# Kernel optimization log

Measured on AMD Instinct MI355X. Metric: run time of the kernel, lower is better.

## Reference

```python
import jax, jax.numpy as jnp
import numpy as np

NUM_PARTS = 2
SAMPLE_STEP = 3  # models sample_points(pts, 3, True) as deterministic stride-3 subsampling


def quat_to_rot(q):
    # wxyz quaternion -> 3x3 rotation (same formula as the torch module)
    q = q / jnp.linalg.norm(q)
    a, b, c, d = q[0], q[1], q[2], q[3]
    return jnp.stack([
        1 - 2 * c * c - 2 * d * d, 2 * b * c - 2 * a * d, 2 * a * c + 2 * b * d,
        2 * b * c + 2 * a * d, 1 - 2 * b * b - 2 * d * d, 2 * c * d - 2 * a * b,
        2 * b * d - 2 * a * c, 2 * a * b + 2 * c * d, 1 - 2 * b * b - 2 * c * c,
    ]).reshape(3, 3)


def make_transform(q, t):
    rot = quat_to_rot(q)                      # (3,3)
    top = jnp.concatenate([rot, t], axis=1)   # (3,4)
    bottom = jnp.array([[0.0, 0.0, 0.0, 1.0]], dtype=top.dtype)
    return jnp.concatenate([top, bottom], axis=0)  # (4,4)


def chamfer(x, y):
    # x: (M,4), y: (M,4) homogeneous points; symmetric chamfer of Euclidean cdist
    d2 = jnp.sum(x * x, -1)[:, None] + jnp.sum(y * y, -1)[None, :] - 2.0 * (x @ y.T)
    d = jnp.sqrt(jnp.maximum(d2, 0.0))
    return jnp.mean(jnp.min(d, axis=1)) + jnp.mean(jnp.min(d, axis=0))


def setup_inputs() -> dict:
    key = jax.random.key(0)
    ks = jax.random.split(key, 6)
    N = 24576
    camera_pts = jax.random.normal(ks[0], (NUM_PARTS, N, 3), dtype=jnp.float32)
    cad_pts = jax.random.normal(ks[1], (NUM_PARTS, N, 3), dtype=jnp.float32)
    part_weight = jax.random.uniform(ks[2], (NUM_PARTS + 1,), dtype=jnp.float32)
    rot_quat = jax.random.normal(ks[3], (NUM_PARTS, 4), dtype=jnp.float32)
    tra = jax.random.normal(ks[4], (NUM_PARTS, 3, 1), dtype=jnp.float32)
    joint_axes = jax.random.normal(ks[5], (NUM_PARTS, 2, 4), dtype=jnp.float32)
    return {"camera_pts": camera_pts, "cad_pts": cad_pts, "part_weight": part_weight,
            "rot_quat": rot_quat, "tra": tra, "joint_axes": joint_axes}


def reference(camera_pts, cad_pts, part_weight, rot_quat, tra, joint_axes):
    # stride-3 subsample, then homogenize with a ones column
    scad = cad_pts[:, ::SAMPLE_STEP]      # (P, M, 3)
    scam = camera_pts[:, ::SAMPLE_STEP]   # (P, M, 3)
    ones = jnp.ones(scad.shape[:-1] + (1,), dtype=scad.dtype)
    scad_h = jnp.concatenate([scad, ones], axis=-1)  # (P, M, 4)
    scam_h = jnp.concatenate([scam, ones], axis=-1)  # (P, M, 4)

    transforms = jax.vmap(make_transform)(rot_quat, tra)        # (P, 4, 4)
    cad_base = jnp.einsum('pij,pnj->pni', transforms, scad_h)   # (P, M, 4)

    e_geo_parts = jax.vmap(chamfer)(cad_base, scam_h)           # (P,)
    e_geo = jnp.dot(part_weight[:NUM_PARTS], e_geo_parts)

    diff = transforms[0] @ joint_axes[0].T - transforms[1] @ joint_axes[1].T  # (4, K)
    e_kin = jax.nn.sigmoid(-5.0 * jnp.linalg.norm(diff))

    all_objective = e_geo + part_weight[NUM_PARTS] * e_kin
    return all_objective, e_kin, jax.lax.stop_gradient(transforms)
```

## Files before the change

### kernel.cpp

```cpp
#include <hip/hip_runtime.h>
#include <math.h>

#define NS 8192
#define NPTS 24576
#define YSPLIT 16
#define YTILE 512
#define BX 256
#define XPT 4
#define XB (NS / (BX * XPT))


__global__ void prep_kernel(const float* __restrict__ rot_quat,
                            const float* __restrict__ tra,
                            const float* __restrict__ joint_axes,
                            float* __restrict__ ws, float* __restrict__ out) {
    if (threadIdx.x == 0) {
        float T[2][16];
        for (int p = 0; p < 2; ++p) {
            float a = rot_quat[p * 4 + 0], b = rot_quat[p * 4 + 1];
            float c = rot_quat[p * 4 + 2], d = rot_quat[p * 4 + 3];
            float inv = rsqrtf(a * a + b * b + c * c + d * d);
            a *= inv; b *= inv; c *= inv; d *= inv;
            float* t = T[p];
            t[0]  = 1.f - 2.f * c * c - 2.f * d * d;
            t[1]  = 2.f * b * c - 2.f * a * d;
            t[2]  = 2.f * a * c + 2.f * b * d;
            t[3]  = tra[p * 3 + 0];
            t[4]  = 2.f * b * c + 2.f * a * d;
            t[5]  = 1.f - 2.f * b * b - 2.f * d * d;
            t[6]  = 2.f * c * d - 2.f * a * b;
            t[7]  = tra[p * 3 + 1];
            t[8]  = 2.f * b * d - 2.f * a * c;
            t[9]  = 2.f * a * b + 2.f * c * d;
            t[10] = 1.f - 2.f * b * b - 2.f * c * c;
            t[11] = tra[p * 3 + 2];
            t[12] = 0.f; t[13] = 0.f; t[14] = 0.f; t[15] = 1.f;
            for (int k = 0; k < 16; ++k) {
                ws[4 + p * 16 + k] = t[k];
                out[2 + p * 16 + k] = t[k];
            }
        }
        float ss = 0.f;
        for (int i = 0; i < 4; ++i) {
            for (int j = 0; j < 2; ++j) {
                float d0 = 0.f, d1 = 0.f;
                for (int k = 0; k < 4; ++k) {
                    d0 += T[0][i * 4 + k] * joint_axes[0 * 8 + j * 4 + k];
                    d1 += T[1][i * 4 + k] * joint_axes[1 * 8 + j * 4 + k];
                }
                float df = d0 - d1;
                ss += df * df;
            }
        }
        float nrm = sqrtf(ss);
        float ek = 1.f / (1.f + expf(5.f * nrm));
        ws[36] = ek;
        out[1] = ek;
        ws[0] = 0.f; ws[1] = 0.f; ws[2] = 0.f; ws[3] = 0.f;
    }
}

__global__ void pack_kernel(const float* __restrict__ cam_pts,
                            const float* __restrict__ cad_pts,
                            const float* __restrict__ ws,
                            float4* __restrict__ pts) {
    int gid = blockIdx.x * blockDim.x + threadIdx.x;
    if (gid >= 2 * NS) return;
    int p = gid >> 13;
    int i = gid & (NS - 1);
    const float* T = ws + 4 + p * 16;
    int base = p * NPTS * 3 + i * 9;
    float x = cad_pts[base], y = cad_pts[base + 1], z = cad_pts[base + 2];
    float q0 = T[0] * x + T[1] * y + T[2]  * z + T[3];
    float q1 = T[4] * x + T[5] * y + T[6]  * z + T[7];
    float q2 = T[8] * x + T[9] * y + T[10] * z + T[11];
    pts[p * NS + i] = make_float4(q0, q1, q2, q0 * q0 + q1 * q1 + q2 * q2);
    float cx = cam_pts[base], cy = cam_pts[base + 1], cz = cam_pts[base + 2];
    pts[2 * NS + p * NS + i] = make_float4(cx, cy, cz, cx * cx + cy * cy + cz * cz);
}

__global__ __launch_bounds__(BX) void chamfer_kernel(const float4* __restrict__ pts,
                                                     float* __restrict__ partial) {
    int combo = blockIdx.y;
    int p   = combo >> 1;
    int dir = combo & 1;
    const float4* X = pts + (dir == 0 ? p * NS : 2 * NS + p * NS);
    const float4* Y = pts + (dir == 0 ? 2 * NS + p * NS : p * NS);
    int ys = blockIdx.z;
    int xb = blockIdx.x;

    __shared__ float4 sy[YTILE];

    int xbase = xb * (BX * XPT) + threadIdx.x;
    float m0[XPT], m1[XPT], m2[XPT], s[XPT], dmin[XPT];
#pragma unroll
    for (int k = 0; k < XPT; ++k) {
        float4 v = X[xbase + k * BX];
        m0[k] = -2.f * v.x;
        m1[k] = -2.f * v.y;
        m2[k] = -2.f * v.z;
        s[k]  = v.w;
        dmin[k] = 3.4e38f;
    }

    int ybase = ys * YTILE;
    sy[threadIdx.x]       = Y[ybase + threadIdx.x];
    sy[threadIdx.x + BX]  = Y[ybase + BX + threadIdx.x];
    __syncthreads();

#pragma unroll 4
    for (int j = 0; j < YTILE; ++j) {
        float4 y = sy[j];
#pragma unroll
        for (int k = 0; k < XPT; ++k) {
            float d = s[k] + y.w;
            d = fmaf(m0[k], y.x, d);
            d = fmaf(m1[k], y.y, d);
            d = fmaf(m2[k], y.z, d);
            dmin[k] = fminf(dmin[k], d);
        }
    }

#pragma unroll
    for (int k = 0; k < XPT; ++k) {
        partial[combo * (YSPLIT * NS) + ys * NS + xbase + k * BX] = dmin[k];
    }
}

__global__ void reduce_kernel(const float* __restrict__ partial,
                              float* __restrict__ accum) {
    int combo = blockIdx.y;
    int x = blockIdx.x * 256 + threadIdx.x;
    const float* p = partial + combo * (YSPLIT * NS) + x;
    float m = p[0];
#pragma unroll
    for (int ysi = 1; ysi < YSPLIT; ++ysi) m = fminf(m, p[ysi * NS]);
    float d = sqrtf(fmaxf(m, 0.f));
#pragma unroll
    for (int off = 32; off > 0; off >>= 1) d += __shfl_down(d, off, 64);
    __shared__ float sm[4];
    int wid = threadIdx.x >> 6;
    if ((threadIdx.x & 63) == 0) sm[wid] = d;
    __syncthreads();
    if (threadIdx.x == 0) {
        float sum = sm[0] + sm[1] + sm[2] + sm[3];
        atomicAdd(&accum[combo], sum);
    }
}

__global__ void finalize_kernel(const float* __restrict__ ws,
                                const float* __restrict__ pw,
                                float* __restrict__ out) {
    if (threadIdx.x == 0) {
        float e0 = (ws[0] + ws[1]) * (1.f / NS);
        float e1 = (ws[2] + ws[3]) * (1.f / NS);
        float e_geo = pw[0] * e0 + pw[1] * e1;
        out[0] = e_geo + pw[2] * ws[36];
    }
}

extern "C" void kernel_launch(void* const* d_in, const int* in_sizes, int n_in,
                              void* d_out, int out_size, void* d_ws, size_t ws_size,
                              hipStream_t stream) {
    const float* cam = (const float*)d_in[0];
    const float* cad = (const float*)d_in[1];
    const float* pw  = (const float*)d_in[2];
    const float* rq  = (const float*)d_in[3];
    const float* tr  = (const float*)d_in[4];
    const float* ja  = (const float*)d_in[5];
    float* out = (float*)d_out;
    float* ws  = (float*)d_ws;
    float4* pts = (float4*)(ws + 64);
    float* partial = ws + 64 + 16 * NS;

    prep_kernel<<<1, 64, 0, stream>>>(rq, tr, ja, ws, out);
    pack_kernel<<<(2 * NS) / 256, 256, 0, stream>>>(cam, cad, ws, pts);
    dim3 cg(XB, 4, YSPLIT);
    chamfer_kernel<<<cg, BX, 0, stream>>>(pts, partial);
    reduce_kernel<<<dim3(NS / 256, 4), 256, 0, stream>>>(partial, ws);
    finalize_kernel<<<1, 64, 0, stream>>>(ws, pw, out);
}
```

Measured before the change: 101.2 us.

## Fuse prep and pack into chamfer kernel and fold finalize into reduce

Drops the separate prep, pack and finalize launches. Each chamfer block now builds its transform itself, gathers the strided raw points directly, and applies the transform on the fly. The reduce kernel uses an atomic ticket counter so the last block writes the final objective. The inner loop also moves the x-norm term out of the per-pair distance and processes two y points per iteration. This cuts launch overhead and the round trip through global memory, at the cost of redundant transform and gather work in every block. The accumulators and ticket counter are zeroed in the fused kernel, so correctness depends on that kernel finishing before the reduce kernel starts, which stream ordering provides.

```diff
diff --git a/kernel.cpp b/kernel.cpp
--- a/kernel.cpp
+++ b/kernel.cpp
@@ -9,153 +9,163 @@
 #define XPT 4
 #define XB (NS / (BX * XPT))
 
+#define PARTIAL_OFF 131136
 
-__global__ void prep_kernel(const float* __restrict__ rot_quat,
-                            const float* __restrict__ tra,
-                            const float* __restrict__ joint_axes,
-                            float* __restrict__ ws, float* __restrict__ out) {
-    if (threadIdx.x == 0) {
-        float T[2][16];
-        for (int p = 0; p < 2; ++p) {
-            float a = rot_quat[p * 4 + 0], b = rot_quat[p * 4 + 1];
-            float c = rot_quat[p * 4 + 2], d = rot_quat[p * 4 + 3];
-            float inv = rsqrtf(a * a + b * b + c * c + d * d);
-            a *= inv; b *= inv; c *= inv; d *= inv;
-            float* t = T[p];
-            t[0]  = 1.f - 2.f * c * c - 2.f * d * d;
-            t[1]  = 2.f * b * c - 2.f * a * d;
-            t[2]  = 2.f * a * c + 2.f * b * d;
-            t[3]  = tra[p * 3 + 0];
-            t[4]  = 2.f * b * c + 2.f * a * d;
-            t[5]  = 1.f - 2.f * b * b - 2.f * d * d;
-            t[6]  = 2.f * c * d - 2.f * a * b;
-            t[7]  = tra[p * 3 + 1];
-            t[8]  = 2.f * b * d - 2.f * a * c;
-            t[9]  = 2.f * a * b + 2.f * c * d;
-            t[10] = 1.f - 2.f * b * b - 2.f * c * c;
-            t[11] = tra[p * 3 + 2];
-            t[12] = 0.f; t[13] = 0.f; t[14] = 0.f; t[15] = 1.f;
-            for (int k = 0; k < 16; ++k) {
-                ws[4 + p * 16 + k] = t[k];
-                out[2 + p * 16 + k] = t[k];
-            }
+__device__ __forceinline__ void make_T12(const float* __restrict__ rq,
+                                         const float* __restrict__ tra,
+                                         int p, float* T) {
+    float a = rq[p * 4 + 0], b = rq[p * 4 + 1];
+    float c = rq[p * 4 + 2], d = rq[p * 4 + 3];
+    float inv = rsqrtf(a * a + b * b + c * c + d * d);
+    a *= inv; b *= inv; c *= inv; d *= inv;
+    T[0]  = 1.f - 2.f * c * c - 2.f * d * d;
+    T[1]  = 2.f * b * c - 2.f * a * d;
+    T[2]  = 2.f * a * c + 2.f * b * d;
+    T[3]  = tra[p * 3 + 0];
+    T[4]  = 2.f * b * c + 2.f * a * d;
+    T[5]  = 1.f - 2.f * b * b - 2.f * d * d;
+    T[6]  = 2.f * c * d - 2.f * a * b;
+    T[7]  = tra[p * 3 + 1];
+    T[8]  = 2.f * b * d - 2.f * a * c;
+    T[9]  = 2.f * a * b + 2.f * c * d;
+    T[10] = 1.f - 2.f * b * b - 2.f * c * c;
+    T[11] = tra[p * 3 + 2];
+}
+
+__global__ __launch_bounds__(BX) void chamfer_fused(
+    const float* __restrict__ cam, const float* __restrict__ cad,
+    const float* __restrict__ rq,  const float* __restrict__ tr,
+    const float* __restrict__ ja,
+    float* __restrict__ ws, float* __restrict__ out)
+{
+    int combo = blockIdx.y;
+    int p   = combo >> 1;
+    int dir = combo & 1;
+
+    float T[12];
+    make_T12(rq, tr, p, T);
+
+    if (blockIdx.x == 0 && blockIdx.y == 0 && blockIdx.z == 0 && threadIdx.x == 0) {
+        float TT[2][16];
+        for (int q = 0; q < 2; ++q) {
+            make_T12(rq, tr, q, TT[q]);
+            TT[q][12] = 0.f; TT[q][13] = 0.f; TT[q][14] = 0.f; TT[q][15] = 1.f;
+            for (int k = 0; k < 16; ++k) out[2 + q * 16 + k] = TT[q][k];
         }
         float ss = 0.f;
         for (int i = 0; i < 4; ++i) {
             for (int j = 0; j < 2; ++j) {
                 float d0 = 0.f, d1 = 0.f;
                 for (int k = 0; k < 4; ++k) {
-                    d0 += T[0][i * 4 + k] * joint_axes[0 * 8 + j * 4 + k];
-                    d1 += T[1][i * 4 + k] * joint_axes[1 * 8 + j * 4 + k];
+                    d0 += TT[0][i * 4 + k] * ja[0 * 8 + j * 4 + k];
+                    d1 += TT[1][i * 4 + k] * ja[1 * 8 + j * 4 + k];
                 }
                 float df = d0 - d1;
                 ss += df * df;
             }
         }
-        float nrm = sqrtf(ss);
-        float ek = 1.f / (1.f + expf(5.f * nrm));
+        float ek = 1.f / (1.f + expf(5.f * sqrtf(ss)));
         ws[36] = ek;
         out[1] = ek;
         ws[0] = 0.f; ws[1] = 0.f; ws[2] = 0.f; ws[3] = 0.f;
+        *(int*)(ws + 40) = 0;
+    }
+
+    int xbase = blockIdx.x * (BX * XPT) + threadIdx.x;
+    const float* xsrc = (dir == 0 ? cad : cam) + p * NPTS * 3;
+    float m0[XPT], m1[XPT], m2[XPT], s[XPT], dmin[XPT];
+#pragma unroll
+    for (int k = 0; k < XPT; ++k) {
+        int i = xbase + k * BX;
+        const float* sp = xsrc + i * 9;
+        float x = sp[0], y = sp[1], z = sp[2];
+        if (dir == 0) {
+            float tx = T[0] * x + T[1] * y + T[2]  * z + T[3];
+            float ty = T[4] * x + T[5] * y + T[6]  * z + T[7];
+            float tz = T[8] * x + T[9] * y + T[10] * z + T[11];
+            x = tx; y = ty; z = tz;
+        }
+        m0[k] = -2.f * x; m1[k] = -2.f * y; m2[k] = -2.f * z;
+        s[k]  = x * x + y * y + z * z;
+        dmin[k] = 3.4e38f;
+    }
+
+    __shared__ float4 sy[YTILE];
+    const float* ysrc = (dir == 0 ? cam : cad) + p * NPTS * 3;
+    int ybase = blockIdx.z * YTILE;
+#pragma unroll
+    for (int t = 0; t < YTILE / BX; ++t) {
+        int i = ybase + t * BX + threadIdx.x;
+        const float* sp = ysrc + i * 9;
+        float x = sp[0], y = sp[1], z = sp[2];
+        if (dir == 1) {
+            float tx = T[0] * x + T[1] * y + T[2]  * z + T[3];
+            float ty = T[4] * x + T[5] * y + T[6]  * z + T[7];
+            float tz = T[8] * x + T[9] * y + T[10] * z + T[11];
+            x = tx; y = ty; z = tz;
+        }
+        sy[t * BX + threadIdx.x] = make_float4(x, y, z, x * x + y * y + z * z);
+    }
+    __syncthreads();
+
+#pragma unroll 4
+    for (int j = 0; j < YTILE; j += 2) {
+        float4 ya = sy[j];
+        float4 yb = sy[j + 1];
+#pragma unroll
+        for (int k = 0; k < XPT; ++k) {
+            float da = fmaf(m0[k], ya.x, ya.w);
+            da = fmaf(m1[k], ya.y, da);
+            da = fmaf(m2[k], ya.z, da);
+            float db = fmaf(m0[k], yb.x, yb.w);
+            db = fmaf(m1[k], yb.y, db);
+            db = fmaf(m2[k], yb.z, db);
+            dmin[k] = fminf(dmin[k], fminf(da, db));
+        }
+    }
+
+    float* partial = ws + PARTIAL_OFF + combo * (YSPLIT * NS) + blockIdx.z * NS;
+#pragma unroll
+    for (int k = 0; k < XPT; ++k) {
+        partial[xbase + k * BX] = s[k] + dmin[k];
     }
 }
 
-__global__ void pack_kernel(const float* __restrict__ cam_pts,
-                            const float* __restrict__ cad_pts,
-                            const float* __restrict__ ws,
-                            float4* __restrict__ pts) {
-    int gid = blockIdx.x * blockDim.x + threadIdx.x;
-    if (gid >= 2 * NS) return;
-    int p = gid >> 13;
-    int i = gid & (NS - 1);
-    const float* T = ws + 4 + p * 16;
-    int base = p * NPTS * 3 + i * 9;
-    float x = cad_pts[base], y = cad_pts[base + 1], z = cad_pts[base + 2];
-    float q0 = T[0] * x + T[1] * y + T[2]  * z + T[3];
-    float q1 = T[4] * x + T[5] * y + T[6]  * z + T[7];
-    float q2 = T[8] * x + T[9] * y + T[10] * z + T[11];
-    pts[p * NS + i] = make_float4(q0, q1, q2, q0 * q0 + q1 * q1 + q2 * q2);
-    float cx = cam_pts[base], cy = cam_pts[base + 1], cz = cam_pts[base + 2];
-    pts[2 * NS + p * NS + i] = make_float4(cx, cy, cz, cx * cx + cy * cy + cz * cz);
-}
-
-__global__ __launch_bounds__(BX) void chamfer_kernel(const float4* __restrict__ pts,
-                                                     float* __restrict__ partial) {
-    int combo = blockIdx.y;
-    int p   = combo >> 1;
-    int dir = combo & 1;
-    const float4* X = pts + (dir == 0 ? p * NS : 2 * NS + p * NS);
-    const float4* Y = pts + (dir == 0 ? 2 * NS + p * NS : p * NS);
-    int ys = blockIdx.z;
-    int xb = blockIdx.x;
-
-    __shared__ float4 sy[YTILE];
-
-    int xbase = xb * (BX * XPT) + threadIdx.x;
-    float m0[XPT], m1[XPT], m2[XPT], s[XPT], dmin[XPT];
-#pragma unroll
-    for (int k = 0; k < XPT; ++k) {
-        float4 v = X[xbase + k * BX];
-        m0[k] = -2.f * v.x;
-        m1[k] = -2.f * v.y;
-        m2[k] = -2.f * v.z;
-        s[k]  = v.w;
-        dmin[k] = 3.4e38f;
-    }
-
-    int ybase = ys * YTILE;
-    sy[threadIdx.x]       = Y[ybase + threadIdx.x];
-    sy[threadIdx.x + BX]  = Y[ybase + BX + threadIdx.x];
-    __syncthreads();
-
-#pragma unroll 4
-    for (int j = 0; j < YTILE; ++j) {
-        float4 y = sy[j];
-#pragma unroll
-        for (int k = 0; k < XPT; ++k) {
-            float d = s[k] + y.w;
-            d = fmaf(m0[k], y.x, d);
-            d = fmaf(m1[k], y.y, d);
-            d = fmaf(m2[k], y.z, d);
-            dmin[k] = fminf(dmin[k], d);
-        }
-    }
-
-#pragma unroll
-    for (int k = 0; k < XPT; ++k) {
-        partial[combo * (YSPLIT * NS) + ys * NS + xbase + k * BX] = dmin[k];
-    }
-}
-
-__global__ void reduce_kernel(const float* __restrict__ partial,
-                              float* __restrict__ accum) {
+__global__ __launch_bounds__(256) void reduce_final(
+    float* __restrict__ ws, const float* __restrict__ pw,
+    float* __restrict__ out)
+{
     int combo = blockIdx.y;
     int x = blockIdx.x * 256 + threadIdx.x;
-    const float* p = partial + combo * (YSPLIT * NS) + x;
+    const float* p = ws + PARTIAL_OFF + combo * (YSPLIT * NS) + x;
     float m = p[0];
 #pragma unroll
     for (int ysi = 1; ysi < YSPLIT; ++ysi) m = fminf(m, p[ysi * NS]);
     float d = sqrtf(fmaxf(m, 0.f));
 #pragma unroll
     for (int off = 32; off > 0; off >>= 1) d += __shfl_down(d, off, 64);
+
     __shared__ float sm[4];
+    __shared__ bool last;
     int wid = threadIdx.x >> 6;
     if ((threadIdx.x & 63) == 0) sm[wid] = d;
     __syncthreads();
     if (threadIdx.x == 0) {
         float sum = sm[0] + sm[1] + sm[2] + sm[3];
-        atomicAdd(&accum[combo], sum);
+        atomicAdd(&ws[combo], sum);
+        __threadfence();
+        int t = atomicAdd((int*)(ws + 40), 1);
+        last = (t == 4 * (NS / 256) - 1);
     }
-}
-
-__global__ void finalize_kernel(const float* __restrict__ ws,
-                                const float* __restrict__ pw,
-                                float* __restrict__ out) {
-    if (threadIdx.x == 0) {
-        float e0 = (ws[0] + ws[1]) * (1.f / NS);
-        float e1 = (ws[2] + ws[3]) * (1.f / NS);
-        float e_geo = pw[0] * e0 + pw[1] * e1;
-        out[0] = e_geo + pw[2] * ws[36];
+    __syncthreads();
+    if (last && threadIdx.x == 0) {
+        float a0 = atomicAdd(&ws[0], 0.f);
+        float a1 = atomicAdd(&ws[1], 0.f);
+        float a2 = atomicAdd(&ws[2], 0.f);
+        float a3 = atomicAdd(&ws[3], 0.f);
+        float e0 = (a0 + a1) * (1.f / NS);
+        float e1 = (a2 + a3) * (1.f / NS);
+        out[0] = pw[0] * e0 + pw[1] * e1 + pw[2] * ws[36];
     }
 }
 
@@ -170,13 +180,8 @@
     const float* ja  = (const float*)d_in[5];
     float* out = (float*)d_out;
     float* ws  = (float*)d_ws;
-    float4* pts = (float4*)(ws + 64);
-    float* partial = ws + 64 + 16 * NS;
 
-    prep_kernel<<<1, 64, 0, stream>>>(rq, tr, ja, ws, out);
-    pack_kernel<<<(2 * NS) / 256, 256, 0, stream>>>(cam, cad, ws, pts);
     dim3 cg(XB, 4, YSPLIT);
-    chamfer_kernel<<<cg, BX, 0, stream>>>(pts, partial);
-    reduce_kernel<<<dim3(NS / 256, 4), 256, 0, stream>>>(partial, ws);
-    finalize_kernel<<<1, 64, 0, stream>>>(ws, pw, out);
+    chamfer_fused<<<cg, BX, 0, stream>>>(cam, cad, rq, tr, ja, ws, out);
+    reduce_final<<<dim3(NS / 256, 4), 256, 0, stream>>>(ws, pw, out);
 }
```

Result: faster. 94.21 us, median of 2 (-6.9%).
